# Optimization experiments

Hardware: AMD Instinct MI355X
Metric: run time of the kernel (lower is better)

The kernel has to match this reference:

```python
import jax, jax.numpy as jnp
import numpy as np

N = 6144      # nodes
DIN = 65      # input_dim (1 time + 64 space coords)
DOUT = 65     # output_dim per head
H = 4         # nheads
EPS = 1e-7
MIN = 1e-15
# curvature c = 1 throughout (MultiHeadGraphAttentionLayer hardcodes curvature=1)

def arcosh(z):
    return jnp.log(z + jnp.sqrt(jnp.maximum(z * z - 1.0, 0.0)))

def hyp_proj(u):
    # project onto hyperboloid: recompute time coord
    y = u[..., 1:]
    t = jnp.sqrt(1.0 + jnp.sum(y * y, -1, keepdims=True))
    return jnp.concatenate([t, y], -1)

def expmap0(u):
    v = u[..., 1:]
    n = jnp.maximum(jnp.linalg.norm(v, axis=-1, keepdims=True), MIN)
    return jnp.concatenate([jnp.cosh(n), jnp.sinh(n) * v / n], -1)

def logmap0(x):
    y = x[..., 1:]
    n = jnp.maximum(jnp.linalg.norm(y, axis=-1, keepdims=True), MIN)
    t = jnp.maximum(x[..., :1], 1.0 + EPS)
    return jnp.concatenate([jnp.zeros_like(t), arcosh(t) * y / n], -1)

def hyp_linear(x, W):
    # HypLinear (use_bias=False, eval mode): mobius_matvec = exp0(log0(x) @ W^T), then proj
    return hyp_proj(expmap0(logmap0(x) @ W.T))

def to_poincare(x):
    return x[..., 1:] / (x[..., :1] + 1.0)

def to_hyperboloid(p):
    s = jnp.sum(p * p, -1, keepdims=True)
    return jnp.concatenate([1.0 + s, 2.0 * p], -1) / jnp.maximum(1.0 - s, MIN)

def mobius_half(v):
    # 0.5 (x) v  (mobius scalar multiplication, c=1)
    n = jnp.maximum(jnp.linalg.norm(v, axis=-1, keepdims=True), MIN)
    return jnp.tanh(0.5 * jnp.arctanh(jnp.minimum(n, 1.0 - EPS))) * v / n

def head(x, adj_t, Wa, Wd, Wo):
    att = hyp_linear(x, Wa)   # [N, DOUT]
    red = hyp_linear(x, Wd)   # [N, DOUT]
    # pairwise hyperboloid sqdist via Minkowski inner product (negate time coord)
    am = att.at[:, 0].multiply(-1.0)
    theta = jnp.maximum(-(am @ att.T), 1.0 + EPS)          # [N, N]
    S = jnp.minimum(arcosh(theta) ** 2, 50.0)
    # coef[i, j] = -adj[j, i] * sqdist for incoming edges (mask = adj^T)
    coef = jnp.where(adj_t > 0.01, -adj_t * S, 0.0)
    # F.normalize along incoming-edge axis (zeros don't change the L2 norm)
    a = coef / jnp.maximum(jnp.linalg.norm(coef, axis=-1, keepdims=True), 1e-12)
    pv = to_poincare(red)                                   # [N, DOUT-1]
    lam = 2.0 / jnp.maximum(1.0 - jnp.sum(pv * pv, -1), MIN)  # conformal factors [N]
    num = (a * lam[None, :]) @ pv                           # [N, DOUT-1]
    den = jnp.sum(jnp.abs(a) * (lam - 1.0)[None, :], -1, keepdims=True)
    m = mobius_half(num / jnp.maximum(den, MIN))            # mobius midpoint
    return hyp_linear(to_hyperboloid(m), Wo)                # [N, DOUT]

def reference(x, adj, W_att, W_data, W_out, W_lin):
    adj_t = adj.T
    hs = jnp.stack([head(x, adj_t, W_att[h], W_data[h], W_out[h]) for h in range(H)], axis=1)  # [N, H, DOUT]
    p = to_poincare(hs).reshape(x.shape[0], -1)             # PoincareBall.concat -> [N, H*(DOUT-1)]
    return hyp_linear(to_hyperboloid(p), W_lin)             # [N, H*DOUT]

def setup_inputs():
    key = jax.random.key(0)
    ks = jax.random.split(key, 8)
    sp = 0.1 * jax.random.normal(ks[0], (N, DIN - 1), jnp.float32)
    x = jnp.concatenate([jnp.sqrt(1.0 + jnp.sum(sp * sp, -1, keepdims=True)), sp], -1)
    adj = (jax.random.uniform(ks[1], (N, N)) < 32.0 / N).astype(jnp.float32)
    adj = jnp.maximum(adj, jnp.eye(N, dtype=jnp.float32))  # every node >=1 incoming edge
    def xavier(k, shape):
        b = (6.0 / (shape[0] + shape[1])) ** 0.5
        return jax.random.uniform(k, shape, jnp.float32, -b, b)
    W_att = jnp.stack([xavier(jax.random.fold_in(ks[2], h), (DOUT, DIN)) for h in range(H)])
    W_data = jnp.stack([xavier(jax.random.fold_in(ks[3], h), (DOUT, DIN)) for h in range(H)])
    W_out = jnp.stack([xavier(jax.random.fold_in(ks[4], h), (DOUT, DOUT)) for h in range(H)])
    W_lin = xavier(ks[5], (H * DOUT, H * (DOUT - 1) + 1))
    return {"x": x, "adj": adj, "W_att": W_att, "W_data": W_data, "W_out": W_out, "W_lin": W_lin}
```

## Files before the change

kernel.cpp:

```cpp
#include <hip/hip_runtime.h>
#include <math.h>

#define N 6144
#define H 4
#define CAP 128
#define MINF 1e-15f
#define ONE_EPS  1.0000001192092896f
#define ONE_MEPS 0.9999998807907104f

__device__ __forceinline__ float wave_reduce_sum(float v) {
    v += __shfl_xor(v, 32, 64);
    v += __shfl_xor(v, 16, 64);
    v += __shfl_xor(v, 8, 64);
    v += __shfl_xor(v, 4, 64);
    v += __shfl_xor(v, 2, 64);
    v += __shfl_xor(v, 1, 64);
    return v;
}

__device__ __forceinline__ float arcosh_f(float z) {
    return logf(z + sqrtf(fmaxf(z * z - 1.0f, 0.0f)));
}

__global__ void k_prep(const float* __restrict__ x, float* __restrict__ lmv,
                       const float* __restrict__ W_att, const float* __restrict__ W_data,
                       const float* __restrict__ W_out, const float* __restrict__ Wl,
                       float* __restrict__ Bp, float* __restrict__ Bo,
                       float* __restrict__ WlT, int* __restrict__ cnt) {
    int b = blockIdx.x;
    if (b < 1536) {
        int i = b * 4 + (threadIdx.x >> 6);
        int lane = threadIdx.x & 63;
        float y = x[i * 65 + 1 + lane];
        float ss = wave_reduce_sum(y * y);
        float n = fmaxf(sqrtf(ss), MINF);
        float t = fmaxf(x[i * 65], ONE_EPS);
        lmv[i * 64 + lane] = arcosh_f(t) * y / n;
    } else if (b < 1728) {
        int tid = (b - 1536) * 256 + threadIdx.x;
        int m = tid >> 12;
        int r = tid & 4095;
        int k = r >> 6, o = r & 63;
        const float* src;
        if (m < 4) src = W_att + m * 65 * 65;
        else if (m < 8) src = W_data + (m - 4) * 65 * 65;
        else src = W_out + (m - 8) * 65 * 65;
        float val = src[(1 + o) * 65 + (1 + k)];
        if (m < 8) Bp[m * 4096 + k * 64 + o] = val;
        else Bo[(m - 8) * 4096 + k * 64 + o] = val;
    } else if (b < 1808) {
        int L = ((b - 1728) * 256 + threadIdx.x) * 4;
        int k = L / 320, o0 = L % 320;
        float v[4];
        #pragma unroll
        for (int q = 0; q < 4; q++) {
            int o = o0 + q;
            v[q] = (o < 259) ? Wl[(size_t)(1 + o) * 257 + 1 + k] : 0.f;
        }
        *(float4*)(WlT + L) = make_float4(v[0], v[1], v[2], v[3]);
    } else {
        cnt[(b - 1808) * 256 + threadIdx.x] = 0;
    }
}

__global__ void __launch_bounds__(256) k_csr_gemm(
        const float* __restrict__ adj, int* __restrict__ cnt, int* __restrict__ idx,
        const float* __restrict__ lmv, const float* __restrict__ Bp,
        float* __restrict__ attv, float2* __restrict__ a0l, float* __restrict__ pv) {
    __shared__ float smem[64 * 65];
    if (blockIdx.x < 768) {
        float (*As)[64] = (float(*)[64])smem;
        float (*Bs)[64] = (float(*)[64])(smem + 1024);
        float (*Cs)[65] = (float(*)[65])smem;
        int my = blockIdx.x / 96;
        int ix = blockIdx.x % 96;
        const float* Bb = Bp + (size_t)my * 4096;
        int i0 = ix * 64;
        int tid = threadIdx.x;
        int tx = tid & 15, ty = tid >> 4;
        float acc[4][4] = {};
        for (int k0 = 0; k0 < 64; k0 += 16) {
            {
                int mm = tid >> 2, kq = tid & 3;
                float4 v = *(const float4*)(lmv + (size_t)(i0 + mm) * 64 + k0 + kq * 4);
                As[kq * 4 + 0][mm] = v.x;
                As[kq * 4 + 1][mm] = v.y;
                As[kq * 4 + 2][mm] = v.z;
                As[kq * 4 + 3][mm] = v.w;
            }
            {
                int kk = tid >> 4, o4 = tid & 15;
                float4 bvv = *(const float4*)(Bb + (k0 + kk) * 64 + o4 * 4);
                *(float4*)&Bs[kk][o4 * 4] = bvv;
            }
            __syncthreads();
            #pragma unroll
            for (int kk = 0; kk < 16; kk++) {
                float4 av = *(const float4*)&As[kk][ty * 4];
                float4 bv = *(const float4*)&Bs[kk][tx * 4];
                float a[4] = {av.x, av.y, av.z, av.w};
                float b[4] = {bv.x, bv.y, bv.z, bv.w};
                #pragma unroll
                for (int r = 0; r < 4; r++)
                    #pragma unroll
                    for (int c = 0; c < 4; c++) acc[r][c] += a[r] * b[c];
            }
            __syncthreads();
        }
        #pragma unroll
        for (int r = 0; r < 4; r++)
            #pragma unroll
            for (int c = 0; c < 4; c++)
                Cs[ty * 4 + r][tx * 4 + c] = acc[r][c];
        __syncthreads();
        int w = tid >> 6, lane = tid & 63;
        bool isAtt = my < 4;
        int h = my & 3;
        #pragma unroll 1
        for (int r = 0; r < 16; r++) {
            int row = w * 16 + r;
            int i = i0 + row;
            float u = Cs[row][lane];
            float nn = fmaxf(sqrtf(wave_reduce_sum(u * u)), MINF);
            if (isAtt) {
                float sha = sinhf(nn);
                attv[((size_t)h * N + i) * 64 + lane] = sha * u / nn;
                if (lane == 0) a0l[h * N + i].x = coshf(nn);
            } else {
                float shd = sinhf(nn), chd = coshf(nn);
                float pvd = (shd * u / nn) / (chd + 1.0f);
                pv[((size_t)h * N + i) * 64 + lane] = pvd;
                float sp = wave_reduce_sum(pvd * pvd);
                if (lane == 0) a0l[h * N + i].y = 2.0f / fmaxf(1.0f - sp, MINF);
            }
        }
    } else {
        const float4* a4 = (const float4*)adj;
        const unsigned STRIDE = 1048576u;
        unsigned e0 = (blockIdx.x - 768) * 256 + threadIdx.x;
        float4 v0 = a4[e0];
        float4 v1 = a4[e0 + STRIDE];
        #pragma unroll 1
        for (int it = 0; it < 9; it++) {
            float4 vn;
            if (it < 7) vn = a4[e0 + (unsigned)(it + 2) * STRIDE];
            unsigned base = (e0 + (unsigned)it * STRIDE) * 4u;
            float vals[4] = {v0.x, v0.y, v0.z, v0.w};
            #pragma unroll
            for (int q = 0; q < 4; q++) {
                if (vals[q] > 0.01f) {
                    unsigned t = base + q;
                    int j = t / N;
                    int i = t % N;
                    int pos = atomicAdd(&cnt[i], 1);
                    if (pos < CAP) idx[i * CAP + pos] = j;
                }
            }
            v0 = v1;
            v1 = vn;
        }
    }
}

__global__ void __launch_bounds__(256) k_attn(
        const int* __restrict__ cnt, const int* __restrict__ idx,
        const float* __restrict__ attv, const float2* __restrict__ a0l,
        const float* __restrict__ pv, float* __restrict__ lm2) {
    __shared__ float wls[4][CAP];
    __shared__ int jls[4][CAP];
    int w = threadIdx.x >> 6, lane = threadIdx.x & 63;
    int i = blockIdx.x * 4 + w;
    int h = blockIdx.y;
    const float* attvh = attv + (size_t)h * N * 64;
    const float* pvh = pv + (size_t)h * N * 64;
    const float2* a0lh = a0l + (size_t)h * N;

    int c = lane & 3;
    float4 aireg[4];
    #pragma unroll
    for (int q = 0; q < 4; q++)
        aireg[q] = *(const float4*)(attvh + (size_t)i * 64 + q * 16 + c * 4);
    float ai0 = a0lh[i].x;
    int nn = min(cnt[i], CAP);

    float accd = 0.f, accss = 0.f;
    for (int base = 0; base < nn; base += 16) {
        int t = base + (lane >> 2);
        bool act = t < nn;
        int j = act ? idx[i * CAP + t] : i;
        float2 al = a0lh[j];
        float d = 0.f;
        #pragma unroll
        for (int q = 0; q < 4; q++) {
            float4 b = *(const float4*)(attvh + (size_t)j * 64 + q * 16 + c * 4);
            float4 a = aireg[q];
            d += a.x * b.x + a.y * b.y + a.z * b.z + a.w * b.w;
        }
        d += __shfl_xor(d, 1, 64);
        d += __shfl_xor(d, 2, 64);
        float theta = fmaxf(ai0 * al.x - d, ONE_EPS);
        float ar = arcosh_f(theta);
        float S = fminf(ar * ar, 50.0f);
        if (!act) S = 0.f;
        if (c == 0) {
            accd += S * (al.y - 1.0f);
            accss += S * S;
            wls[w][t] = S * al.y;
            jls[w][t] = j;
        }
    }
    accd = wave_reduce_sum(accd);
    accss = wave_reduce_sum(accss);
    float nrm = fmaxf(sqrtf(accss), 1e-12f);
    float den = fmaxf(accd / nrm, MINF);
    float scl = 1.0f / (nrm * den);

    float accn = 0.f;
    #pragma unroll 4
    for (int t = 0; t < nn; t++) {
        int j = jls[w][t];
        float wq = wls[w][t];
        accn = fmaf(wq, pvh[(size_t)j * 64 + lane], accn);
    }
    float v = -scl * accn;
    float nv = fmaxf(sqrtf(wave_reduce_sum(v * v)), MINF);
    float nc = fminf(nv, ONE_MEPS);
    float mh = tanhf(0.5f * atanhf(nc));
    float md = mh * v / nv;
    float s = wave_reduce_sum(md * md);
    float Dh = fmaxf(1.0f - s, MINF);
    float hb0 = (1.0f + s) / Dh;
    float hbv = 2.0f * md / Dh;
    float nh = fmaxf(2.0f * sqrtf(s) / Dh, MINF);
    float t2 = fmaxf(hb0, ONE_EPS);
    lm2[((size_t)h * N + i) * 64 + lane] = arcosh_f(t2) * hbv / nh;
}

__global__ void __launch_bounds__(256) k_gemm_out(
        const float* __restrict__ lm2, const float* __restrict__ Bo,
        float* __restrict__ p) {
    __shared__ float As[16][64];
    __shared__ float Bs[16][64];
    __shared__ float Cs[64][65];
    int h = blockIdx.y;
    const float* Ab = lm2 + (size_t)h * N * 64;
    const float* Bb = Bo + (size_t)h * 4096;
    int i0 = blockIdx.x * 64;
    int tid = threadIdx.x;
    int tx = tid & 15, ty = tid >> 4;
    float acc[4][4] = {};
    for (int k0 = 0; k0 < 64; k0 += 16) {
        {
            int mm = tid >> 2, kq = tid & 3;
            float4 v = *(const float4*)(Ab + (size_t)(i0 + mm) * 64 + k0 + kq * 4);
            As[kq * 4 + 0][mm] = v.x;
            As[kq * 4 + 1][mm] = v.y;
            As[kq * 4 + 2][mm] = v.z;
            As[kq * 4 + 3][mm] = v.w;
        }
        {
            int kk = tid >> 4, o4 = tid & 15;
            float4 bvv = *(const float4*)(Bb + (k0 + kk) * 64 + o4 * 4);
            *(float4*)&Bs[kk][o4 * 4] = bvv;
        }
        __syncthreads();
        #pragma unroll
        for (int kk = 0; kk < 16; kk++) {
            float4 av = *(const float4*)&As[kk][ty * 4];
            float4 bv = *(const float4*)&Bs[kk][tx * 4];
            float a[4] = {av.x, av.y, av.z, av.w};
            float b[4] = {bv.x, bv.y, bv.z, bv.w};
            #pragma unroll
            for (int r = 0; r < 4; r++)
                #pragma unroll
                for (int c = 0; c < 4; c++) acc[r][c] += a[r] * b[c];
        }
        __syncthreads();
    }
    #pragma unroll
    for (int r = 0; r < 4; r++)
        #pragma unroll
        for (int c = 0; c < 4; c++)
            Cs[ty * 4 + r][tx * 4 + c] = acc[r][c];
    __syncthreads();
    int w = tid >> 6, lane = tid & 63;
    #pragma unroll 1
    for (int r16 = 0; r16 < 16; r16++) {
        int row = w * 16 + r16;
        int i = i0 + row;
        float u = Cs[row][lane];
        float nv = fmaxf(sqrtf(wave_reduce_sum(u * u)), MINF);
        float sh = sinhf(nv), ch = coshf(nv);
        p[(size_t)i * 256 + h * 64 + lane] = (sh * u / nv) / (ch + 1.0f);
    }
}

__global__ void k_final_logmap(const float* __restrict__ p, float* __restrict__ lmF) {
    __shared__ float part[4];
    int i = blockIdx.x;
    int t = threadIdx.x;
    int w = t >> 6;
    float pd = p[(size_t)i * 256 + t];
    float ss = wave_reduce_sum(pd * pd);
    if ((t & 63) == 0) part[w] = ss;
    __syncthreads();
    float s = part[0] + part[1] + part[2] + part[3];
    float Dh = fmaxf(1.0f - s, MINF);
    float hb0 = (1.0f + s) / Dh;
    float hbv = 2.0f * pd / Dh;
    float n = fmaxf(2.0f * sqrtf(s) / Dh, MINF);
    float tt = fmaxf(hb0, ONE_EPS);
    lmF[(size_t)i * 256 + t] = arcosh_f(tt) * hbv / n;
}

__global__ void __launch_bounds__(256) k_final_gemm(
        const float* __restrict__ A, const float* __restrict__ WlT,
        float* __restrict__ U) {
    __shared__ float As[16][64];
    __shared__ float Bs[16][64];
    int i0 = blockIdx.x * 64;
    int o0 = blockIdx.y * 64;
    int tid = threadIdx.x;
    int tx = tid & 15, ty = tid >> 4;
    float acc[4][4] = {};
    for (int k0 = 0; k0 < 256; k0 += 16) {
        {
            int mm = tid >> 2;
            int kq = tid & 3;
            const float4 v = *(const float4*)(A + (size_t)(i0 + mm) * 256 + k0 + kq * 4);
            As[kq * 4 + 0][mm] = v.x;
            As[kq * 4 + 1][mm] = v.y;
            As[kq * 4 + 2][mm] = v.z;
            As[kq * 4 + 3][mm] = v.w;
        }
        {
            int kk = tid >> 4, o4 = tid & 15;
            *(float4*)&Bs[kk][o4 * 4] =
                *(const float4*)(WlT + (size_t)(k0 + kk) * 320 + o0 + o4 * 4);
        }
        __syncthreads();
        #pragma unroll
        for (int kk = 0; kk < 16; kk++) {
            float4 av = *(const float4*)&As[kk][ty * 4];
            float4 bv = *(const float4*)&Bs[kk][tx * 4];
            float a[4] = {av.x, av.y, av.z, av.w};
            float b[4] = {bv.x, bv.y, bv.z, bv.w};
            #pragma unroll
            for (int r = 0; r < 4; r++)
                #pragma unroll
                for (int c = 0; c < 4; c++) acc[r][c] += a[r] * b[c];
        }
        __syncthreads();
    }
    #pragma unroll
    for (int r = 0; r < 4; r++) {
        int i = i0 + ty * 4 + r;
        #pragma unroll
        for (int c = 0; c < 4; c++) {
            int o = o0 + tx * 4 + c;
            if (o < 259) U[(size_t)i * 260 + o] = acc[r][c];
        }
    }
}

__global__ void k_final_epilogue(const float* __restrict__ U, float* __restrict__ out) {
    __shared__ float part[4];
    int i = blockIdx.x;
    int t = threadIdx.x;
    float a = U[(size_t)i * 260 + t];
    float b = (t < 3) ? U[(size_t)i * 260 + 256 + t] : 0.f;
    float ss = wave_reduce_sum(a * a + b * b);
    if ((t & 63) == 0) part[t >> 6] = ss;
    __syncthreads();
    ss = part[0] + part[1] + part[2] + part[3];
    float nv = fmaxf(sqrtf(ss), MINF);
    float sh = sinhf(nv);
    float scale = sh / nv;
    out[(size_t)i * 260 + 1 + t] = scale * a;
    if (t < 3) out[(size_t)i * 260 + 257 + t] = scale * b;
    if (t == 0) out[(size_t)i * 260] = sqrtf(1.0f + sh * sh);
}

extern "C" void kernel_launch(void* const* d_in, const int* in_sizes, int n_in,
                              void* d_out, int out_size, void* d_ws, size_t ws_size,
                              hipStream_t stream) {
    const float* x = (const float*)d_in[0];
    const float* adj = (const float*)d_in[1];
    const float* W_att = (const float*)d_in[2];
    const float* W_data = (const float*)d_in[3];
    const float* W_out = (const float*)d_in[4];
    const float* W_lin = (const float*)d_in[5];
    float* out = (float*)d_out;

    char* ws = (char*)d_ws;
    size_t off = 0;
    auto alloc = [&](size_t bytes) {
        void* ptr = ws + off;
        off += (bytes + 255) & ~(size_t)255;
        return ptr;
    };
    int* cnt = (int*)alloc((size_t)N * 4);
    int* idx = (int*)alloc((size_t)N * CAP * 4);
    float* lmv = (float*)alloc((size_t)N * 64 * 4);
    float* attv = (float*)alloc((size_t)H * N * 64 * 4);
    float2* a0l = (float2*)alloc((size_t)H * N * 8);
    float* pvb = (float*)alloc((size_t)H * N * 64 * 4);
    float* lm2 = (float*)alloc((size_t)H * N * 64 * 4);
    float* Bp = (float*)alloc((size_t)8 * 4096 * 4);
    float* Bo = (float*)alloc((size_t)4 * 4096 * 4);
    float* WlT = (float*)alloc((size_t)256 * 320 * 4);
    float* U = (float*)alloc((size_t)N * 260 * 4);
    float* lmF = attv;
    float* p = pvb;

    k_prep<<<1832, 256, 0, stream>>>(x, lmv, W_att, W_data, W_out, W_lin,
                                     Bp, Bo, WlT, cnt);
    k_csr_gemm<<<4864, 256, 0, stream>>>(adj, cnt, idx, lmv, Bp, attv, a0l, pvb);
    k_attn<<<dim3(N / 4, H), 256, 0, stream>>>(cnt, idx, attv, a0l, pvb, lm2);
    k_gemm_out<<<dim3(N / 64, H), 256, 0, stream>>>(lm2, Bo, p);
    k_final_logmap<<<N, 256, 0, stream>>>(p, lmF);
    k_final_gemm<<<dim3(N / 64, 5), 256, 0, stream>>>(lmF, WlT, U);
    k_final_epilogue<<<N, 256, 0, stream>>>(U, out);
}
```

Before: 336.1 us.

## Fuse output-head GEMM with logmap and final GEMM with epilogue

Merges the per-head output GEMM with the Poincaré-concat logmap so that one block handles all four heads for 32 rows, keeps them in shared memory, and writes lmF directly. It also merges the final GEMM with the expmap epilogue by keeping all 260 output columns in LDS. This removes two kernel launches and the global round trips of the p and U intermediates. In exchange the grids are smaller (192 blocks), shared memory per block is larger, and the global loads become scalar where they were float4, which may lower occupancy and memory efficiency.

After: 421.2 us. 1.25x slower.

```diff
diff --git a/kernel.cpp b/kernel.cpp
--- a/kernel.cpp
+++ b/kernel.cpp
@@ -236,149 +236,150 @@
     lm2[((size_t)h * N + i) * 64 + lane] = arcosh_f(t2) * hbv / nh;
 }
 
-__global__ void __launch_bounds__(256) k_gemm_out(
+__global__ void __launch_bounds__(256) k_out_fused(
         const float* __restrict__ lm2, const float* __restrict__ Bo,
-        float* __restrict__ p) {
-    __shared__ float As[16][64];
+        float* __restrict__ lmF) {
+    __shared__ float As[16][32];
     __shared__ float Bs[16][64];
-    __shared__ float Cs[64][65];
-    int h = blockIdx.y;
-    const float* Ab = lm2 + (size_t)h * N * 64;
-    const float* Bb = Bo + (size_t)h * 4096;
-    int i0 = blockIdx.x * 64;
+    __shared__ float Ps[32][257];
+    int i0 = blockIdx.x * 32;
     int tid = threadIdx.x;
     int tx = tid & 15, ty = tid >> 4;
-    float acc[4][4] = {};
-    for (int k0 = 0; k0 < 64; k0 += 16) {
-        {
-            int mm = tid >> 2, kq = tid & 3;
-            float4 v = *(const float4*)(Ab + (size_t)(i0 + mm) * 64 + k0 + kq * 4);
-            As[kq * 4 + 0][mm] = v.x;
-            As[kq * 4 + 1][mm] = v.y;
-            As[kq * 4 + 2][mm] = v.z;
-            As[kq * 4 + 3][mm] = v.w;
-        }
-        {
-            int kk = tid >> 4, o4 = tid & 15;
-            float4 bvv = *(const float4*)(Bb + (k0 + kk) * 64 + o4 * 4);
-            *(float4*)&Bs[kk][o4 * 4] = bvv;
-        }
+    for (int h = 0; h < H; h++) {
+        const float* Ab = lm2 + (size_t)h * N * 64;
+        const float* Bb = Bo + (size_t)h * 4096;
+        float acc[2][4] = {};
+        for (int k0 = 0; k0 < 64; k0 += 16) {
+            {
+                int mm = tid & 31, kb = (tid >> 5) * 2;
+                As[kb + 0][mm] = Ab[(size_t)(i0 + mm) * 64 + k0 + kb + 0];
+                As[kb + 1][mm] = Ab[(size_t)(i0 + mm) * 64 + k0 + kb + 1];
+            }
+            {
+                int o = tid & 63, kb = (tid >> 6) * 4;
+                Bs[kb + 0][o] = Bb[(k0 + kb + 0) * 64 + o];
+                Bs[kb + 1][o] = Bb[(k0 + kb + 1) * 64 + o];
+                Bs[kb + 2][o] = Bb[(k0 + kb + 2) * 64 + o];
+                Bs[kb + 3][o] = Bb[(k0 + kb + 3) * 64 + o];
+            }
+            __syncthreads();
+            #pragma unroll
+            for (int kk = 0; kk < 16; kk++) {
+                float4 bv = *(const float4*)&Bs[kk][tx * 4];
+                float a0 = As[kk][ty * 2 + 0];
+                float a1 = As[kk][ty * 2 + 1];
+                acc[0][0] += a0 * bv.x; acc[0][1] += a0 * bv.y;
+                acc[0][2] += a0 * bv.z; acc[0][3] += a0 * bv.w;
+                acc[1][0] += a1 * bv.x; acc[1][1] += a1 * bv.y;
+                acc[1][2] += a1 * bv.z; acc[1][3] += a1 * bv.w;
+            }
+            __syncthreads();
+        }
+        #pragma unroll
+        for (int r = 0; r < 2; r++)
+            #pragma unroll
+            for (int c2 = 0; c2 < 4; c2++)
+                Ps[ty * 2 + r][h * 64 + tx * 4 + c2] = acc[r][c2];
         __syncthreads();
-        #pragma unroll
-        for (int kk = 0; kk < 16; kk++) {
-            float4 av = *(const float4*)&As[kk][ty * 4];
-            float4 bv = *(const float4*)&Bs[kk][tx * 4];
-            float a[4] = {av.x, av.y, av.z, av.w};
-            float b[4] = {bv.x, bv.y, bv.z, bv.w};
-            #pragma unroll
-            for (int r = 0; r < 4; r++)
-                #pragma unroll
-                for (int c = 0; c < 4; c++) acc[r][c] += a[r] * b[c];
-        }
-        __syncthreads();
-    }
-    #pragma unroll
-    for (int r = 0; r < 4; r++)
-        #pragma unroll
-        for (int c = 0; c < 4; c++)
-            Cs[ty * 4 + r][tx * 4 + c] = acc[r][c];
-    __syncthreads();
+    }
     int w = tid >> 6, lane = tid & 63;
     #pragma unroll 1
-    for (int r16 = 0; r16 < 16; r16++) {
-        int row = w * 16 + r16;
+    for (int r = 0; r < 8; r++) {
+        int row = w * 8 + r;
         int i = i0 + row;
-        float u = Cs[row][lane];
-        float nv = fmaxf(sqrtf(wave_reduce_sum(u * u)), MINF);
-        float sh = sinhf(nv), ch = coshf(nv);
-        p[(size_t)i * 256 + h * 64 + lane] = (sh * u / nv) / (ch + 1.0f);
-    }
-}
-
-__global__ void k_final_logmap(const float* __restrict__ p, float* __restrict__ lmF) {
-    __shared__ float part[4];
-    int i = blockIdx.x;
-    int t = threadIdx.x;
-    int w = t >> 6;
-    float pd = p[(size_t)i * 256 + t];
-    float ss = wave_reduce_sum(pd * pd);
-    if ((t & 63) == 0) part[w] = ss;
-    __syncthreads();
-    float s = part[0] + part[1] + part[2] + part[3];
-    float Dh = fmaxf(1.0f - s, MINF);
-    float hb0 = (1.0f + s) / Dh;
-    float hbv = 2.0f * pd / Dh;
-    float n = fmaxf(2.0f * sqrtf(s) / Dh, MINF);
-    float tt = fmaxf(hb0, ONE_EPS);
-    lmF[(size_t)i * 256 + t] = arcosh_f(tt) * hbv / n;
-}
-
-__global__ void __launch_bounds__(256) k_final_gemm(
+        float pr[4];
+        float sp[4];
+        #pragma unroll
+        for (int h = 0; h < 4; h++) {
+            float u = Ps[row][h * 64 + lane];
+            float nv = fmaxf(sqrtf(wave_reduce_sum(u * u)), MINF);
+            float sh = sinhf(nv), ch = coshf(nv);
+            float pd = (sh * u / nv) / (ch + 1.0f);
+            pr[h] = pd;
+            sp[h] = wave_reduce_sum(pd * pd);
+        }
+        float s = ((sp[0] + sp[1]) + sp[2]) + sp[3];
+        float Dh = fmaxf(1.0f - s, MINF);
+        float hb0 = (1.0f + s) / Dh;
+        float nrm = fmaxf(2.0f * sqrtf(s) / Dh, MINF);
+        float tt = fmaxf(hb0, ONE_EPS);
+        float fac = arcosh_f(tt);
+        #pragma unroll
+        for (int h = 0; h < 4; h++) {
+            float hbv = 2.0f * pr[h] / Dh;
+            lmF[(size_t)i * 256 + h * 64 + lane] = fac * hbv / nrm;
+        }
+    }
+}
+
+__global__ void __launch_bounds__(256) k_final_fused2(
         const float* __restrict__ A, const float* __restrict__ WlT,
-        float* __restrict__ U) {
-    __shared__ float As[16][64];
+        float* __restrict__ out) {
+    __shared__ float As[16][32];
     __shared__ float Bs[16][64];
-    int i0 = blockIdx.x * 64;
-    int o0 = blockIdx.y * 64;
+    __shared__ float Us[32][261];
+    int i0 = blockIdx.x * 32;
     int tid = threadIdx.x;
     int tx = tid & 15, ty = tid >> 4;
-    float acc[4][4] = {};
-    for (int k0 = 0; k0 < 256; k0 += 16) {
-        {
-            int mm = tid >> 2;
-            int kq = tid & 3;
-            const float4 v = *(const float4*)(A + (size_t)(i0 + mm) * 256 + k0 + kq * 4);
-            As[kq * 4 + 0][mm] = v.x;
-            As[kq * 4 + 1][mm] = v.y;
-            As[kq * 4 + 2][mm] = v.z;
-            As[kq * 4 + 3][mm] = v.w;
-        }
-        {
-            int kk = tid >> 4, o4 = tid & 15;
-            *(float4*)&Bs[kk][o4 * 4] =
-                *(const float4*)(WlT + (size_t)(k0 + kk) * 320 + o0 + o4 * 4);
-        }
+    for (int co = 0; co < 5; co++) {
+        int o0 = co * 64;
+        float acc[2][4] = {};
+        for (int k0 = 0; k0 < 256; k0 += 16) {
+            {
+                int mm = tid & 31, kb = (tid >> 5) * 2;
+                As[kb + 0][mm] = A[(size_t)(i0 + mm) * 256 + k0 + kb + 0];
+                As[kb + 1][mm] = A[(size_t)(i0 + mm) * 256 + k0 + kb + 1];
+            }
+            {
+                int o = tid & 63, kb = (tid >> 6) * 4;
+                Bs[kb + 0][o] = WlT[(size_t)(k0 + kb + 0) * 320 + o0 + o];
+                Bs[kb + 1][o] = WlT[(size_t)(k0 + kb + 1) * 320 + o0 + o];
+                Bs[kb + 2][o] = WlT[(size_t)(k0 + kb + 2) * 320 + o0 + o];
+                Bs[kb + 3][o] = WlT[(size_t)(k0 + kb + 3) * 320 + o0 + o];
+            }
+            __syncthreads();
+            #pragma unroll
+            for (int kk = 0; kk < 16; kk++) {
+                float4 bv = *(const float4*)&Bs[kk][tx * 4];
+                float a0 = As[kk][ty * 2 + 0];
+                float a1 = As[kk][ty * 2 + 1];
+                acc[0][0] += a0 * bv.x; acc[0][1] += a0 * bv.y;
+                acc[0][2] += a0 * bv.z; acc[0][3] += a0 * bv.w;
+                acc[1][0] += a1 * bv.x; acc[1][1] += a1 * bv.y;
+                acc[1][2] += a1 * bv.z; acc[1][3] += a1 * bv.w;
+            }
+            __syncthreads();
+        }
+        #pragma unroll
+        for (int r = 0; r < 2; r++)
+            #pragma unroll
+            for (int c2 = 0; c2 < 4; c2++) {
+                int oc = o0 + tx * 4 + c2;
+                if (oc < 260) Us[ty * 2 + r][oc] = acc[r][c2];
+            }
         __syncthreads();
-        #pragma unroll
-        for (int kk = 0; kk < 16; kk++) {
-            float4 av = *(const float4*)&As[kk][ty * 4];
-            float4 bv = *(const float4*)&Bs[kk][tx * 4];
-            float a[4] = {av.x, av.y, av.z, av.w};
-            float b[4] = {bv.x, bv.y, bv.z, bv.w};
-            #pragma unroll
-            for (int r = 0; r < 4; r++)
-                #pragma unroll
-                for (int c = 0; c < 4; c++) acc[r][c] += a[r] * b[c];
-        }
-        __syncthreads();
-    }
-    #pragma unroll
-    for (int r = 0; r < 4; r++) {
-        int i = i0 + ty * 4 + r;
-        #pragma unroll
-        for (int c = 0; c < 4; c++) {
-            int o = o0 + tx * 4 + c;
-            if (o < 259) U[(size_t)i * 260 + o] = acc[r][c];
-        }
-    }
-}
-
-__global__ void k_final_epilogue(const float* __restrict__ U, float* __restrict__ out) {
-    __shared__ float part[4];
-    int i = blockIdx.x;
-    int t = threadIdx.x;
-    float a = U[(size_t)i * 260 + t];
-    float b = (t < 3) ? U[(size_t)i * 260 + 256 + t] : 0.f;
-    float ss = wave_reduce_sum(a * a + b * b);
-    if ((t & 63) == 0) part[t >> 6] = ss;
-    __syncthreads();
-    ss = part[0] + part[1] + part[2] + part[3];
-    float nv = fmaxf(sqrtf(ss), MINF);
-    float sh = sinhf(nv);
-    float scale = sh / nv;
-    out[(size_t)i * 260 + 1 + t] = scale * a;
-    if (t < 3) out[(size_t)i * 260 + 257 + t] = scale * b;
-    if (t == 0) out[(size_t)i * 260] = sqrtf(1.0f + sh * sh);
+    }
+    int w = tid >> 6, lane = tid & 63;
+    #pragma unroll 1
+    for (int r = 0; r < 8; r++) {
+        int row = w * 8 + r;
+        int i = i0 + row;
+        float u0 = Us[row][lane];
+        float u1 = Us[row][64 + lane];
+        float u2 = Us[row][128 + lane];
+        float u3 = Us[row][192 + lane];
+        float u4 = (lane < 3) ? Us[row][256 + lane] : 0.f;
+        float ss = wave_reduce_sum(u0 * u0 + u1 * u1 + u2 * u2 + u3 * u3 + u4 * u4);
+        float nv = fmaxf(sqrtf(ss), MINF);
+        float sh = sinhf(nv);
+        float sc = sh / nv;
+        out[(size_t)i * 260 + 1 + lane]   = sc * u0;
+        out[(size_t)i * 260 + 65 + lane]  = sc * u1;
+        out[(size_t)i * 260 + 129 + lane] = sc * u2;
+        out[(size_t)i * 260 + 193 + lane] = sc * u3;
+        if (lane < 3) out[(size_t)i * 260 + 257 + lane] = sc * u4;
+        if (lane == 0) out[(size_t)i * 260] = sqrtf(1.0f + sh * sh);
+    }
 }
 
 extern "C" void kernel_launch(void* const* d_in, const int* in_sizes, int n_in,
@@ -409,16 +410,12 @@
     float* Bp = (float*)alloc((size_t)8 * 4096 * 4);
     float* Bo = (float*)alloc((size_t)4 * 4096 * 4);
     float* WlT = (float*)alloc((size_t)256 * 320 * 4);
-    float* U = (float*)alloc((size_t)N * 260 * 4);
     float* lmF = attv;
-    float* p = pvb;
 
     k_prep<<<1832, 256, 0, stream>>>(x, lmv, W_att, W_data, W_out, W_lin,
                                      Bp, Bo, WlT, cnt);
     k_csr_gemm<<<4864, 256, 0, stream>>>(adj, cnt, idx, lmv, Bp, attv, a0l, pvb);
     k_attn<<<dim3(N / 4, H), 256, 0, stream>>>(cnt, idx, attv, a0l, pvb, lm2);
-    k_gemm_out<<<dim3(N / 64, H), 256, 0, stream>>>(lm2, Bo, p);
-    k_final_logmap<<<N, 256, 0, stream>>>(p, lmF);
-    k_final_gemm<<<dim3(N / 64, 5), 256, 0, stream>>>(lmF, WlT, U);
-    k_final_epilogue<<<N, 256, 0, stream>>>(U, out);
-}
+    k_out_fused<<<N / 32, 256, 0, stream>>>(lm2, Bo, lmF);
+    k_final_fused2<<<N / 32, 256, 0, stream>>>(lmF, WlT, out);
+}
```
